# Kernel optimization log

Hardware: AMD Instinct MI355X
Metric: run time of the kernel (lower is better)

## Reference

```python
import jax, jax.numpy as jnp
import numpy as np
import math

N = 100000
D = 128       # input_dim
DK = 32       # d_k
H = 4         # heads
DV = D // H   # d_v = 32
DFF = 512     # 4 * input_dim
EPS = 1e-5


def layer_norm(x, g, b):
    mu = jnp.mean(x, axis=-1, keepdims=True)
    var = jnp.var(x, axis=-1, keepdims=True)
    return (x - mu) * jax.lax.rsqrt(var + EPS) * g + b


def setup_inputs() -> dict:
    key = jax.random.key(0)
    ks = jax.random.split(key, 10)
    x = jax.random.normal(ks[0], (N, D), dtype=jnp.float32)
    neighbor_index = jax.random.randint(ks[1], (N, 4), 0, N)
    # xavier-ish scaled params
    w_q = jax.random.normal(ks[2], (H, D, DK), dtype=jnp.float32) * math.sqrt(2.0 / (D + DK))
    w_k = jax.random.normal(ks[3], (H, 5, D, DK), dtype=jnp.float32) * math.sqrt(2.0 / (D + DK))
    w_v = jax.random.normal(ks[4], (H, 5, D, DV), dtype=jnp.float32) * math.sqrt(2.0 / (D + DV))
    W1 = jax.random.normal(ks[5], (D, DFF), dtype=jnp.float32) * math.sqrt(1.0 / D)
    b1 = jnp.zeros((DFF,), dtype=jnp.float32)
    W2 = jax.random.normal(ks[6], (DFF, D), dtype=jnp.float32) * math.sqrt(1.0 / DFF)
    b2 = jnp.zeros((D,), dtype=jnp.float32)
    g1 = jnp.ones((D,), dtype=jnp.float32)
    beta1 = jnp.zeros((D,), dtype=jnp.float32)
    g2 = jnp.ones((D,), dtype=jnp.float32)
    beta2 = jnp.zeros((D,), dtype=jnp.float32)
    return {"x": x, "neighbor_index": neighbor_index, "w_q": w_q, "w_k": w_k,
            "w_v": w_v, "W1": W1, "b1": b1, "W2": W2, "b2": b2,
            "g1": g1, "beta1": beta1, "g2": g2, "beta2": beta2}


def attention(x, neighbor_index, w_q, w_k, w_v):
    # gather the 4 typed neighbors and prepend the self node -> (N, 5, D)
    x_nb = jnp.concatenate([x[:, None, :], x[neighbor_index]], axis=1)
    Q = jnp.einsum('nd,hdk->hnk', x, w_q)                 # (H, N, DK)
    K = jnp.einsum('nrd,hrdk->hnrk', x_nb, w_k)           # (H, N, 5, DK)
    V = jnp.einsum('nrd,hrdv->hnrv', x_nb, w_v)           # (H, N, 5, DV)
    A = jnp.einsum('hnk,hnrk->hnr', Q, K) / math.sqrt(DK)
    # NOTE: original torch code applies softmax over dim=1 (the node axis),
    # reproduced faithfully here.
    A = jax.nn.softmax(A, axis=1)
    Z = jnp.einsum('hnr,hnrv->hnv', A, V)                 # (H, N, DV)
    return jnp.transpose(Z, (1, 0, 2)).reshape(x.shape[0], -1)  # (N, H*DV)


def reference(x, neighbor_index, w_q, w_k, w_v, W1, b1, W2, b2, g1, beta1, g2, beta2):
    attn = attention(x, neighbor_index, w_q, w_k, w_v)
    h = layer_norm(x + attn, g1, beta1)
    ffn = jax.nn.relu(h @ W1 + b1) @ W2 + b2
    return layer_norm(h + ffn, g2, beta2)
```

## Files before the change

kernel.cpp:

```cpp
#include <hip/hip_runtime.h>
#include <hip/hip_bf16.h>

typedef unsigned short u16;
typedef __attribute__((ext_vector_type(8))) short short8;
typedef __attribute__((ext_vector_type(4))) float f32x4;
typedef __attribute__((ext_vector_type(4))) float float4v;
typedef __attribute__((ext_vector_type(4))) unsigned short us4;
typedef __attribute__((ext_vector_type(4))) int int4v;

#define NN       100000
#define NWG      782
#define OFF_WK   16384
#define OFF_WV   98304
#define OFF_W1   180224
#define PACK_ELEMS 311296

#define WS_LWS   0u
#define WS_PM    8000000u
#define WS_PS    8000640u
#define WS_MHR   8001280u
#define WS_ISHR  8001408u
#define WS_PK    8001536u
#define WS_XB    8624128u
#define WS_SV    34224128u

#define PWS_PITCH 40
#define PWS_SLICE 1280

static __device__ __forceinline__ float b2f(u16 u){
  unsigned int i = ((unsigned int)u) << 16;
  float f; __builtin_memcpy(&f, &i, 4); return f;
}
static __device__ __forceinline__ u16 f2b(float f){
  unsigned int i; __builtin_memcpy(&i, &f, 4);
  i += 0x7FFFu + ((i >> 16) & 1u);
  return (u16)(i >> 16);
}
static __device__ __forceinline__ f32x4 mfma16(short8 a, short8 b, f32x4 c){
  return __builtin_amdgcn_mfma_f32_16x16x32_bf16(a, b, c, 0, 0, 0);
}
static __device__ __forceinline__ bool detect32(const void* g1){
  return ((const u16*)g1)[0] == 0;
}
static __device__ __forceinline__ float ldf(const void* p, size_t i, bool is32){
  return is32 ? ((const float*)p)[i] : b2f(((const u16*)p)[i]);
}
static __device__ __forceinline__ int swz_wg(int b){
  const int q = NWG >> 3, r = NWG & 7;
  int x = b & 7, i = b >> 3;
  return (x < r ? x*(q+1) : r*(q+1) + (x-r)*q) + i;
}

static __device__ __forceinline__ void stage32k(
    const u16* __restrict__ g, u16* l, int wv, int lane)
{
  #pragma unroll
  for (int k = 0; k < 8; k++){
    int off = k*4096 + wv*1024;
    __builtin_amdgcn_global_load_lds(
        (const __attribute__((address_space(1))) void*)((const char*)g + off + lane*16),
        (__attribute__((address_space(3))) void*)((char*)l + off),
        16, 0, 0);
  }
}

#define VMW16() asm volatile("s_waitcnt vmcnt(16)" ::: "memory")
#define VMW8()  asm volatile("s_waitcnt vmcnt(8)" ::: "memory")
#define VMW0()  asm volatile("s_waitcnt vmcnt(0)" ::: "memory")
#define SBAR()  asm volatile("s_barrier" ::: "memory")
#define PRIO1() __builtin_amdgcn_s_setprio(1)
#define PRIO0() __builtin_amdgcn_s_setprio(0)

__global__ __launch_bounds__(256) void k_prep(
    const void* __restrict__ x, const void* __restrict__ wq,
    const void* __restrict__ wk, const void* __restrict__ wv,
    const void* __restrict__ W1, const void* __restrict__ W2,
    const void* __restrict__ g1, const void* __restrict__ b1,
    const void* __restrict__ b2, const void* __restrict__ be1,
    const void* __restrict__ g2, const void* __restrict__ be2,
    u16* __restrict__ xb, u16* __restrict__ pk, u16* __restrict__ sv)
{
  const bool is32 = detect32(g1);
  {
    size_t i = (size_t)blockIdx.x * 256 + threadIdx.x;
    us4 o;
    if (is32){
      float4v v = ((const float4v*)x)[i];
      o.x = f2b(v.x); o.y = f2b(v.y); o.z = f2b(v.z); o.w = f2b(v.w);
    } else {
      o = ((const us4*)x)[i];
    }
    ((us4*)xb)[i] = o;
  }
  int p = blockIdx.x * 256 + threadIdx.x;
  if (p < PACK_ELEMS){
    float v;
    if (p < OFF_WK){
      int q = p;
      int j = q & 7, lane = (q >> 3) & 63, tk = q >> 9;
      int kb = tk & 3, t = tk >> 2;
      int kd = kb*32 + (lane>>4)*8 + j, nc = t*16 + (lane & 15);
      v = ldf(wq, (size_t)(nc>>5)*4096 + kd*32 + (nc & 31), is32);
    } else if (p < OFF_WV){
      int q = p - OFF_WK; int r = q >> 14; q &= 16383;
      int j = q & 7, lane = (q >> 3) & 63, tk = q >> 9;
      int kb = tk & 3, t = tk >> 2;
      int kd = kb*32 + (lane>>4)*8 + j, nc = t*16 + (lane & 15);
      v = ldf(wk, (size_t)((nc>>5)*5 + r)*4096 + kd*32 + (nc & 31), is32);
    } else if (p < OFF_W1){
      int q = p - OFF_WV; int r = q >> 14; q &= 16383;
      int j = q & 7, lane = (q >> 3) & 63, tk = q >> 9;
      int kb = tk & 3, t = tk >> 2;
      int kd = kb*32 + (lane>>4)*8 + j, nc = t*16 + (lane & 15);
      v = ldf(wv, (size_t)((nc>>5)*5 + r)*4096 + kd*32 + (nc & 31), is32);
    } else {
      int q = p - OFF_W1;
      int j = q & 7, lane = (q >> 3) & 63, rest = q >> 9;
      int pairIdx = rest >> 4, sub = rest & 15;
      int c = pairIdx >> 2, kb2 = pairIdx & 3;
      int half = lane >> 4, mc = lane & 15;
      if (sub < 8){
        int u = sub >> 2, kb = sub & 3;
        int kd = kb*32 + half*8 + j;
        int nc = c*128 + (kb2*2+u)*16 + mc;
        v = ldf(W1, (size_t)kd*512 + nc, is32);
      } else {
        int t = sub - 8;
        int kd = (c*4+kb2)*32 + half*8 + j;
        int nc = t*16 + mc;
        v = ldf(W2, (size_t)kd*128 + nc, is32);
      }
    }
    pk[p] = f2b(v);
  }
  if (blockIdx.x == 0){
    for (int i = threadIdx.x; i < 1152; i += 256){
      const void* src; int off;
      if      (i < 512) { src = b1;  off = i; }
      else if (i < 640) { src = b2;  off = i - 512; }
      else if (i < 768) { src = g1;  off = i - 640; }
      else if (i < 896) { src = be1; off = i - 768; }
      else if (i < 1024){ src = g2;  off = i - 896; }
      else              { src = be2; off = i - 1024; }
      sv[i] = f2b(ldf(src, off, is32));
    }
  }
}

__global__ __launch_bounds__(256, 2) void k_qk(
    const u16* __restrict__ x, const int* __restrict__ nbr,
    const u16* __restrict__ pw, float* __restrict__ lws)
{
  __shared__ __align__(16) u16 sbuf[32768];
  const int tid = threadIdx.x, lane = tid & 63, wv = tid >> 6;
  const int m = lane & 15, quad = lane >> 4;
  const int blk = swz_wg(blockIdx.x);
  const int n0 = blk * 128 + wv * 32;
  const bool act0 = (n0 < NN), act1 = (n0 + 16 < NN);
  const short8* sb8 = (const short8*)sbuf;

  int nd[2][4];
  short8 a2[2][4], a2n[2][4];
  #pragma unroll
  for (int tl = 0; tl < 2; tl++){
    if (!(tl ? act1 : act0)) continue;
    int4v t4 = *(const int4v*)(nbr + (size_t)(n0 + tl*16 + m)*4);
    nd[tl][0]=t4.x; nd[tl][1]=t4.y; nd[tl][2]=t4.z; nd[tl][3]=t4.w;
    const short8* xp = (const short8*)(x + (size_t)(n0 + tl*16 + m) * 128);
    #pragma unroll
    for (int kb = 0; kb < 4; kb++) a2[tl][kb] = xp[kb*4 + quad];
  }

  stage32k(pw, sbuf, wv, lane);
  stage32k(pw + OFF_WK, sbuf + 16384, wv, lane);

  f32x4 q[2][8];
  #pragma unroll
  for (int tl = 0; tl < 2; tl++)
    #pragma unroll
    for (int t = 0; t < 8; t++) q[tl][t] = (f32x4){0.f,0.f,0.f,0.f};

  VMW8(); SBAR();
  PRIO1();
  #pragma unroll
  for (int t = 0; t < 8; t++){
    short8 bfr[4];
    #pragma unroll
    for (int kb = 0; kb < 4; kb++) bfr[kb] = sb8[(t*4+kb)*64 + lane];
    #pragma unroll
    for (int tl = 0; tl < 2; tl++){
      if (!(tl ? act1 : act0)) continue;
      #pragma unroll
      for (int kb = 0; kb < 4; kb++) q[tl][t] = mfma16(a2[tl][kb], bfr[kb], q[tl][t]);
    }
  }
  PRIO0();
  SBAR();
  stage32k(pw + OFF_WK + 16384, sbuf, wv, lane);

  for (int r = 0; r < 5; r++){
    if (r >= 1 && r <= 3) { VMW16(); } else { VMW8(); }
    SBAR();
    const short8* cur = sb8 + ((r+1)&1)*2048;
    if (r < 4){
      #pragma unroll
      for (int tl = 0; tl < 2; tl++){
        if (!(tl ? act1 : act0)) continue;
        const short8* gp = (const short8*)(x + (size_t)nd[tl][r] * 128);
        #pragma unroll
        for (int kb = 0; kb < 4; kb++) a2n[tl][kb] = gp[kb*4 + quad];
      }
    }
    #pragma unroll
    for (int h = 0; h < 4; h++){
      short8 b0[4], b1f[4];
      #pragma unroll
      for (int kb = 0; kb < 4; kb++){
        b0[kb]  = cur[((2*h  )*4+kb)*64 + lane];
        b1f[kb] = cur[((2*h+1)*4+kb)*64 + lane];
      }
      #pragma unroll
      for (int tl = 0; tl < 2; tl++){
        if (!(tl ? act1 : act0)) continue;
        f32x4 k0 = {0.f,0.f,0.f,0.f}, k1 = {0.f,0.f,0.f,0.f};
        PRIO1();
        #pragma unroll
        for (int kb = 0; kb < 4; kb++){
          k0 = mfma16(a2[tl][kb], b0[kb],  k0);
          k1 = mfma16(a2[tl][kb], b1f[kb], k1);
        }
        PRIO0();
        float p[4];
        #pragma unroll
        for (int i = 0; i < 4; i++) p[i] = q[tl][2*h][i]*k0[i] + q[tl][2*h+1][i]*k1[i];
        #pragma unroll
        for (int mask = 1; mask < 16; mask <<= 1){
          #pragma unroll
          for (int i = 0; i < 4; i++) p[i] += __shfl_xor(p[i], mask, 16);
        }
        if (m == 0){
          #pragma unroll
          for (int i = 0; i < 4; i++)
            lws[(size_t)(h*5+r)*NN + n0 + tl*16 + quad*4 + i]
                = p[i] * 0.17677669529663687f;
        }
      }
    }
    if (r < 4){
      #pragma unroll
      for (int tl = 0; tl < 2; tl++)
        #pragma unroll
        for (int kb = 0; kb < 4; kb++) a2[tl][kb] = a2n[tl][kb];
    }
    SBAR();
    if (r <= 2)
      stage32k(pw + OFF_WK + (r+2)*16384, sbuf + ((r+1)&1)*16384, wv, lane);
  }
}

__global__ __launch_bounds__(256) void k_red_part(
    const float* __restrict__ lws, float* __restrict__ pm, float* __restrict__ ps)
{
  const int hr = blockIdx.x >> 3, pb = blockIdx.x & 7;
  const int start = pb * 12500, end = start + 12500;
  const float* v = lws + (size_t)hr * NN;
  __shared__ float red[256];
  float mx = -1e30f;
  for (int i = start + threadIdx.x; i < end; i += 256) mx = fmaxf(mx, v[i]);
  red[threadIdx.x] = mx; __syncthreads();
  for (int s = 128; s > 0; s >>= 1){
    if ((int)threadIdx.x < s) red[threadIdx.x] = fmaxf(red[threadIdx.x], red[threadIdx.x+s]);
    __syncthreads();
  }
  mx = red[0]; __syncthreads();
  float sm = 0.f;
  for (int i = start + threadIdx.x; i < end; i += 256) sm += __expf(v[i] - mx);
  red[threadIdx.x] = sm; __syncthreads();
  for (int s = 128; s > 0; s >>= 1){
    if ((int)threadIdx.x < s) red[threadIdx.x] += red[threadIdx.x+s];
    __syncthreads();
  }
  if (threadIdx.x == 0){ pm[blockIdx.x] = mx; ps[blockIdx.x] = red[0]; }
}

__global__ __launch_bounds__(256, 2) void k_attn_ffn(
    const u16* __restrict__ x, const void* __restrict__ xraw,
    const int* __restrict__ nbr,
    const u16* __restrict__ pw, const float* __restrict__ lws,
    const float* __restrict__ pm, const float* __restrict__ ps,
    const u16* __restrict__ sv, const void* __restrict__ g1raw,
    float* __restrict__ out)
{
  __shared__ __align__(16) u16 sbuf[32768];
  __shared__ __align__(16) u16 upool[5120];
  const int tid = threadIdx.x, lane = tid & 63, wv = tid >> 6;
  const int m = lane & 15, quad = lane >> 4;
  const int blk = swz_wg(blockIdx.x);
  const int n0 = blk * 128 + wv * 32;
  const bool act0 = (n0 < NN), act1 = (n0 + 16 < NN);
  const bool is32 = detect32(g1raw);
  const u16* b1s = sv;
  const u16* b2s = sv + 512;
  const u16* g1s = sv + 640;
  const u16* be1s = sv + 768;
  const u16* g2s = sv + 896;
  const u16* be2s = sv + 1024;
  const short8* sb8 = (const short8*)sbuf;
  const u16* wvp = pw + OFF_WV;
  const u16* wfp = pw + OFF_W1;
  float* attw_w = ((float*)upool) + wv * 640;
  u16*   pws_w  = upool + wv * PWS_SLICE;

  float Mreg = -1e30f, iSreg = 0.f;
  if (lane < 20){
    float M = -1e30f;
    #pragma unroll
    for (int b = 0; b < 8; b++) M = fmaxf(M, pm[lane*8+b]);
    float S = 0.f;
    #pragma unroll
    for (int b = 0; b < 8; b++) S += ps[lane*8+b] * __expf(pm[lane*8+b] - M);
    Mreg = M; iSreg = 1.0f / S;
  }

  for (int j = lane; j < 640; j += 64){
    int tl = j / 320, rem = j - tl*320;
    int r = rem >> 6, h = (rem >> 4) & 3, mm = rem & 15, hr = h*5 + r;
    int node = n0 + tl*16 + mm;
    float Mh = __shfl(Mreg, hr), iSh = __shfl(iSreg, hr);
    attw_w[j] = (node < NN)
        ? __expf(lws[(size_t)hr*NN + node] - Mh) * iSh : 0.f;
  }

  int nd[2][4];
  short8 a2[2][4], a2n[2][4];
  #pragma unroll
  for (int tl = 0; tl < 2; tl++){
    if (!(tl ? act1 : act0)) continue;
    int4v t4 = *(const int4v*)(nbr + (size_t)(n0 + tl*16 + m)*4);
    nd[tl][0]=t4.x; nd[tl][1]=t4.y; nd[tl][2]=t4.z; nd[tl][3]=t4.w;
    const short8* xp = (const short8*)(x + (size_t)(n0 + tl*16 + m) * 128);
    #pragma unroll
    for (int kb = 0; kb < 4; kb++) a2[tl][kb] = xp[kb*4 + quad];
  }

  stage32k(wvp, sbuf, wv, lane);
  stage32k(wvp + 16384, sbuf + 16384, wv, lane);

  f32x4 zacc[2][8];
  #pragma unroll
  for (int tl = 0; tl < 2; tl++)
    #pragma unroll
    for (int t = 0; t < 8; t++) zacc[tl][t] = (f32x4){0.f,0.f,0.f,0.f};

  for (int r = 0; r < 5; r++){
    if (r >= 1) { VMW16(); } else { VMW8(); }
    SBAR();
    const short8* cur = sb8 + (r&1)*2048;
    if (r < 4){
      #pragma unroll
      for (int tl = 0; tl < 2; tl++){
        if (!(tl ? act1 : act0)) continue;
        const short8* gp = (const short8*)(x + (size_t)nd[tl][r] * 128);
        #pragma unroll
        for (int kb = 0; kb < 4; kb++) a2n[tl][kb] = gp[kb*4 + quad];
      }
    }
    #pragma unroll
    for (int t = 0; t < 8; t++){
      short8 bfr[4];
      #pragma unroll
      for (int kb = 0; kb < 4; kb++) bfr[kb] = cur[(t*4+kb)*64 + lane];
      int h = t >> 1;
      #pragma unroll
      for (int tl = 0; tl < 2; tl++){
        if (!(tl ? act1 : act0)) continue;
        f32x4 v = {0.f,0.f,0.f,0.f};
        PRIO1();
        #pragma unroll
        for (int kb = 0; kb < 4; kb++) v = mfma16(a2[tl][kb], bfr[kb], v);
        PRIO0();
        const float* aw = attw_w + tl*320 + (r*4+h)*16;
        #pragma unroll
        for (int i = 0; i < 4; i++) zacc[tl][t][i] += aw[quad*4+i] * v[i];
      }
    }
    if (r < 4){
      #pragma unroll
      for (int tl = 0; tl < 2; tl++)
        #pragma unroll
        for (int kb = 0; kb < 4; kb++) a2[tl][kb] = a2n[tl][kb];
    }
    SBAR();
    {
      int b = r + 2;
      const u16* src = (b < 5) ? wvp + b*16384 : wfp + (b-5)*16384;
      stage32k(src, sbuf + (r&1)*16384, wv, lane);
    }
  }

  float mu[2][4], rs[2][4];
  #pragma unroll
  for (int tl = 0; tl < 2; tl++){
    if (!(tl ? act1 : act0)) continue;
    int rowb = n0 + tl*16;
    #pragma unroll
    for (int t = 0; t < 8; t++)
      #pragma unroll
      for (int i = 0; i < 4; i++)
        zacc[tl][t][i] += ldf(xraw, (size_t)(rowb + quad*4 + i)*128 + t*16 + m, is32);
    float s1[4] = {0,0,0,0}, s2[4] = {0,0,0,0};
    #pragma unroll
    for (int t = 0; t < 8; t++)
      #pragma unroll
      for (int i = 0; i < 4; i++){ float y = zacc[tl][t][i]; s1[i] += y; s2[i] += y*y; }
    #pragma unroll
    for (int mask = 1; mask < 16; mask <<= 1){
      #pragma unroll
      for (int i = 0; i < 4; i++){
        s1[i] += __shfl_xor(s1[i], mask, 16);
        s2[i] += __shfl_xor(s2[i], mask, 16);
      }
    }
    #pragma unroll
    for (int i = 0; i < 4; i++){
      mu[tl][i] = s1[i] * (1.f/128.f);
      float var = s2[i] * (1.f/128.f) - mu[tl][i]*mu[tl][i];
      rs[tl][i] = rsqrtf(var + 1e-5f);
    }
  }

  unsigned int hDp[2][8][2];
  short8 ah[2][4];
  #pragma unroll
  for (int kb = 0; kb < 4; kb++){
    #pragma unroll
    for (int u = 0; u < 2; u++){
      int t = kb*2 + u;
      #pragma unroll
      for (int tl = 0; tl < 2; tl++){
        if (!(tl ? act1 : act0)) continue;
        float gg = b2f(g1s[t*16+m]), bb = b2f(be1s[t*16+m]);
        u16 hv[4];
        #pragma unroll
        for (int i = 0; i < 4; i++){
          hv[i] = f2b((zacc[tl][t][i]-mu[tl][i])*rs[tl][i]*gg + bb);
          pws_w[(tl*16 + quad*4 + i)*PWS_PITCH + u*16 + m] = hv[i];
        }
        hDp[tl][t][0] = (unsigned int)hv[0] | ((unsigned int)hv[1] << 16);
        hDp[tl][t][1] = (unsigned int)hv[2] | ((unsigned int)hv[3] << 16);
      }
    }
    #pragma unroll
    for (int tl = 0; tl < 2; tl++)
      ah[tl][kb] = *(const short8*)(pws_w + (tl*16 + m)*PWS_PITCH + quad*8);
  }

  f32x4 f2acc[2][8];
  #pragma unroll
  for (int tl = 0; tl < 2; tl++)
    #pragma unroll
    for (int t = 0; t < 8; t++) f2acc[tl][t] = (f32x4){0.f,0.f,0.f,0.f};

  for (int s = 0; s < 8; s++){
    if (s < 7) { VMW8(); } else { VMW0(); }
    SBAR();
    const short8* cur = sb8 + ((s+1)&1)*2048;
    const int c = s >> 1, kp = s & 1;
    #pragma unroll
    for (int kb2w = 0; kb2w < 2; kb2w++){
      int kb2 = kp*2 + kb2w;
      const short8* w1f = cur + kb2w*1024;
      const short8* w2f = w1f + 512;
      #pragma unroll
      for (int u = 0; u < 2; u++){
        short8 bfr[4];
        #pragma unroll
        for (int kb = 0; kb < 4; kb++) bfr[kb] = w1f[(u*4+kb)*64 + lane];
        float b1c = b2f(b1s[c*128 + (kb2*2+u)*16 + m]);
        #pragma unroll
        for (int tl = 0; tl < 2; tl++){
          if (!(tl ? act1 : act0)) continue;
          f32x4 g = {0.f,0.f,0.f,0.f};
          PRIO1();
          #pragma unroll
          for (int kb = 0; kb < 4; kb++) g = mfma16(ah[tl][kb], bfr[kb], g);
          PRIO0();
          #pragma unroll
          for (int i = 0; i < 4; i++)
            pws_w[(tl*16 + quad*4 + i)*PWS_PITCH + u*16 + m]
                = f2b(fmaxf(g[i] + b1c, 0.f));
        }
      }
      short8 ag[2];
      #pragma unroll
      for (int tl = 0; tl < 2; tl++)
        ag[tl] = *(const short8*)(pws_w + (tl*16 + m)*PWS_PITCH + quad*8);
      PRIO1();
      #pragma unroll
      for (int t = 0; t < 8; t++){
        short8 bf = w2f[t*64 + lane];
        #pragma unroll
        for (int tl = 0; tl < 2; tl++){
          if (!(tl ? act1 : act0)) continue;
          f2acc[tl][t] = mfma16(ag[tl], bf, f2acc[tl][t]);
        }
      }
      PRIO0();
    }
    SBAR();
    if (s <= 5)
      stage32k(wfp + (s+2)*16384, sbuf + ((s+1)&1)*16384, wv, lane);
  }

  #pragma unroll
  for (int tl = 0; tl < 2; tl++){
    if (!(tl ? act1 : act0)) continue;
    int rowb = n0 + tl*16;
    #pragma unroll
    for (int t = 0; t < 8; t++){
      float b2c = b2f(b2s[t*16 + m]);
      f2acc[tl][t][0] += b2f((u16)(hDp[tl][t][0] & 0xffff)) + b2c;
      f2acc[tl][t][1] += b2f((u16)(hDp[tl][t][0] >> 16))    + b2c;
      f2acc[tl][t][2] += b2f((u16)(hDp[tl][t][1] & 0xffff)) + b2c;
      f2acc[tl][t][3] += b2f((u16)(hDp[tl][t][1] >> 16))    + b2c;
    }
    float s1[4] = {0,0,0,0}, s2[4] = {0,0,0,0};
    #pragma unroll
    for (int t = 0; t < 8; t++)
      #pragma unroll
      for (int i = 0; i < 4; i++){ float y = f2acc[tl][t][i]; s1[i] += y; s2[i] += y*y; }
    #pragma unroll
    for (int mask = 1; mask < 16; mask <<= 1){
      #pragma unroll
      for (int i = 0; i < 4; i++){
        s1[i] += __shfl_xor(s1[i], mask, 16);
        s2[i] += __shfl_xor(s2[i], mask, 16);
      }
    }
    float mu2[4], rs2[4];
    #pragma unroll
    for (int i = 0; i < 4; i++){
      mu2[i] = s1[i] * (1.f/128.f);
      float var = s2[i] * (1.f/128.f) - mu2[i]*mu2[i];
      rs2[i] = rsqrtf(var + 1e-5f);
    }
    #pragma unroll
    for (int t = 0; t < 8; t++){
      float gg = b2f(g2s[t*16+m]), bb = b2f(be2s[t*16+m]);
      #pragma unroll
      for (int i = 0; i < 4; i++)
        out[(size_t)(rowb + quad*4 + i)*128 + t*16 + m] =
            (f2acc[tl][t][i]-mu2[i])*rs2[i]*gg + bb;
    }
  }
}

extern "C" void kernel_launch(void* const* d_in, const int* in_sizes, int n_in,
                              void* d_out, int out_size, void* d_ws, size_t ws_size,
                              hipStream_t stream)
{
  const void* x   = d_in[0];
  const int*  nbr = (const int*)d_in[1];
  const void* wq  = d_in[2];
  const void* wk  = d_in[3];
  const void* wv  = d_in[4];
  const void* W1  = d_in[5];
  const void* b1  = d_in[6];
  const void* W2  = d_in[7];
  const void* b2  = d_in[8];
  const void* g1  = d_in[9];
  const void* be1 = d_in[10];
  const void* g2  = d_in[11];
  const void* be2 = d_in[12];
  float* out = (float*)d_out;

  char* ws = (char*)d_ws;
  float* lws  = (float*)(ws + WS_LWS);
  float* pm   = (float*)(ws + WS_PM);
  float* ps   = (float*)(ws + WS_PS);
  u16*   pk   = (u16*)  (ws + WS_PK);
  u16*   xb   = (u16*)  (ws + WS_XB);
  u16*   sv   = (u16*)  (ws + WS_SV);

  k_prep<<<dim3(12500), dim3(256), 0, stream>>>(x, wq, wk, wv, W1, W2, g1,
                                                b1, b2, be1, g2, be2, xb, pk, sv);
  k_qk<<<dim3(NWG), dim3(256), 0, stream>>>(xb, nbr, pk, lws);
  k_red_part<<<dim3(160), dim3(256), 0, stream>>>(lws, pm, ps);
  k_attn_ffn<<<dim3(NWG), dim3(256), 0, stream>>>(xb, x, nbr, pk, lws, pm, ps,
                                                  sv, g1, out);
}
```

Before: 297.5 us.

## Restructure weight double-buffering to single barrier per stage with one-ahead prefetch

New measurement: 303.9 us. 2.2% more time.

```diff
diff --git a/kernel.cpp b/kernel.cpp
--- a/kernel.cpp
+++ b/kernel.cpp
@@ -18,8 +18,6 @@
 #define WS_LWS   0u
 #define WS_PM    8000000u
 #define WS_PS    8000640u
-#define WS_MHR   8001280u
-#define WS_ISHR  8001408u
 #define WS_PK    8001536u
 #define WS_XB    8624128u
 #define WS_SV    34224128u
@@ -64,10 +62,8 @@
   }
 }
 
-#define VMW16() asm volatile("s_waitcnt vmcnt(16)" ::: "memory")
-#define VMW8()  asm volatile("s_waitcnt vmcnt(8)" ::: "memory")
-#define VMW0()  asm volatile("s_waitcnt vmcnt(0)" ::: "memory")
-#define SBAR()  asm volatile("s_barrier" ::: "memory")
+#define VMW0() asm volatile("s_waitcnt vmcnt(0)" ::: "memory")
+#define SBAR() asm volatile("s_barrier" ::: "memory")
 #define PRIO1() __builtin_amdgcn_s_setprio(1)
 #define PRIO0() __builtin_amdgcn_s_setprio(0)
 
@@ -172,15 +168,15 @@
   }
 
   stage32k(pw, sbuf, wv, lane);
+
+  f32x4 q[2][8];
+  #pragma unroll
+  for (int tl = 0; tl < 2; tl++)
+    #pragma unroll
+    for (int t = 0; t < 8; t++) q[tl][t] = (f32x4){0.f,0.f,0.f,0.f};
+
+  VMW0(); SBAR();
   stage32k(pw + OFF_WK, sbuf + 16384, wv, lane);
-
-  f32x4 q[2][8];
-  #pragma unroll
-  for (int tl = 0; tl < 2; tl++)
-    #pragma unroll
-    for (int t = 0; t < 8; t++) q[tl][t] = (f32x4){0.f,0.f,0.f,0.f};
-
-  VMW8(); SBAR();
   PRIO1();
   #pragma unroll
   for (int t = 0; t < 8; t++){
@@ -195,12 +191,11 @@
     }
   }
   PRIO0();
-  SBAR();
-  stage32k(pw + OFF_WK + 16384, sbuf, wv, lane);
 
   for (int r = 0; r < 5; r++){
-    if (r >= 1 && r <= 3) { VMW16(); } else { VMW8(); }
-    SBAR();
+    VMW0(); SBAR();
+    if (r < 4)
+      stage32k(pw + OFF_WK + (r+1)*16384, sbuf + (r&1)*16384, wv, lane);
     const short8* cur = sb8 + ((r+1)&1)*2048;
     if (r < 4){
       #pragma unroll
@@ -252,9 +247,6 @@
         #pragma unroll
         for (int kb = 0; kb < 4; kb++) a2[tl][kb] = a2n[tl][kb];
     }
-    SBAR();
-    if (r <= 2)
-      stage32k(pw + OFF_WK + (r+2)*16384, sbuf + ((r+1)&1)*16384, wv, lane);
   }
 }
 
@@ -344,7 +336,6 @@
   }
 
   stage32k(wvp, sbuf, wv, lane);
-  stage32k(wvp + 16384, sbuf + 16384, wv, lane);
 
   f32x4 zacc[2][8];
   #pragma unroll
@@ -353,8 +344,12 @@
     for (int t = 0; t < 8; t++) zacc[tl][t] = (f32x4){0.f,0.f,0.f,0.f};
 
   for (int r = 0; r < 5; r++){
-    if (r >= 1) { VMW16(); } else { VMW8(); }
-    SBAR();
+    VMW0(); SBAR();
+    {
+      int b = r + 1;
+      const u16* src = (b < 5) ? wvp + b*16384 : wfp;
+      stage32k(src, sbuf + ((r+1)&1)*16384, wv, lane);
+    }
     const short8* cur = sb8 + (r&1)*2048;
     if (r < 4){
       #pragma unroll
@@ -389,12 +384,6 @@
       for (int tl = 0; tl < 2; tl++)
         #pragma unroll
         for (int kb = 0; kb < 4; kb++) a2[tl][kb] = a2n[tl][kb];
-    }
-    SBAR();
-    {
-      int b = r + 2;
-      const u16* src = (b < 5) ? wvp + b*16384 : wfp + (b-5)*16384;
-      stage32k(src, sbuf + (r&1)*16384, wv, lane);
     }
   }
 
@@ -462,8 +451,9 @@
     for (int t = 0; t < 8; t++) f2acc[tl][t] = (f32x4){0.f,0.f,0.f,0.f};
 
   for (int s = 0; s < 8; s++){
-    if (s < 7) { VMW8(); } else { VMW0(); }
-    SBAR();
+    VMW0(); SBAR();
+    if (s < 7)
+      stage32k(wfp + (s+1)*16384, sbuf + (s&1)*16384, wv, lane);
     const short8* cur = sb8 + ((s+1)&1)*2048;
     const int c = s >> 1, kp = s & 1;
     #pragma unroll
@@ -507,9 +497,6 @@
       }
       PRIO0();
     }
-    SBAR();
-    if (s <= 5)
-      stage32k(wfp + (s+2)*16384, sbuf + ((s+1)&1)*16384, wv, lane);
   }
 
   #pragma unroll
```
